# Performance work log

Measured on AMD Instinct MI355X. Metric: run time of the kernel, lower is better.

Reference implementation:

```python
import jax, jax.numpy as jnp
import numpy as np

N_ENT = 50000
N_EDGE = 500000
H_DIM = 128
N_REL_TAB = 475  # 2*n_rel + 1


def setup_inputs() -> dict:
    key = jax.random.key(0)
    ks = jax.random.split(key, 8)
    scale = 1.0 / np.sqrt(H_DIM)
    return {
        "ent_emb": jax.random.normal(ks[0], (N_ENT, H_DIM), jnp.float32) * scale,
        "rel_emb": jax.random.normal(ks[1], (N_REL_TAB, H_DIM), jnp.float32) * scale,
        "w_edge": jax.random.normal(ks[2], (H_DIM, H_DIM), jnp.float32) * scale,
        "w_node": jax.random.normal(ks[3], (H_DIM, H_DIM), jnp.float32) * scale,
        "w_comp": jax.random.normal(ks[4], (H_DIM, H_DIM), jnp.float32) * scale,
        "src": jax.random.randint(ks[5], (N_EDGE,), 0, N_ENT, jnp.int32),
        "dst": jax.random.randint(ks[6], (N_EDGE,), 0, N_ENT, jnp.int32),
        "rel_id": jax.random.randint(ks[7], (N_EDGE,), 0, N_REL_TAB - 1, jnp.int32),
    }


def _edge_softmax(logits, dst, n_nodes):
    # dgl.ops.edge_softmax: softmax over incoming edges of each destination node
    m = jax.ops.segment_max(logits, dst, num_segments=n_nodes)  # (N,)
    ex = jnp.exp(logits - m[dst])                               # (E,)
    s = jax.ops.segment_sum(ex, dst, num_segments=n_nodes)     # (N,)
    return ex / s[dst]


def _attn_aggregate(msg, key_emb_dst, dst, n_nodes, w):
    # norm = e_dot_v, edge_softmax, weighted scatter-sum, GEMM, Tanh
    logits = jnp.sum(msg * key_emb_dst, axis=-1)                # (E,)
    a = _edge_softmax(logits, dst, n_nodes)                     # (E,)
    neigh = jax.ops.segment_sum(msg * a[:, None], dst, num_segments=n_nodes)  # (N,H)
    return jnp.tanh(neigh @ w)


def reference(ent_emb, rel_emb, w_edge, w_node, w_comp, src, dst, rel_id):
    n = ent_emb.shape[0]
    v = ent_emb[dst]            # (E,H) destination node emb (shared key for all layers)
    u = ent_emb[src]            # (E,H)
    r = rel_emb[rel_id]         # (E,H)

    # EdgeLayer: message = rel emb
    edge_out = _attn_aggregate(r, v, dst, n, w_edge)
    # NodeLayer: message = src node emb (u_dot_v logits, u_mul_e aggregation)
    node_out = _attn_aggregate(u, v, dst, n, w_node)
    # CompLayer (comp_op='add'): message = u + rel emb
    comp_out = _attn_aggregate(u + r, v, dst, n, w_comp)

    return ent_emb + edge_out + node_out + comp_out
```

## Files before the change

kernel.cpp:

```cpp
#include <hip/hip_runtime.h>
#include <math.h>

#define N_ENT   50000
#define N_REL   475
#define N_EDGE  500000
#define HD      128

typedef unsigned int u32;
typedef __attribute__((ext_vector_type(8))) short short8;
typedef __attribute__((ext_vector_type(4))) float f32x4;
typedef __attribute__((ext_vector_type(4))) u32 u32x4;

__device__ __forceinline__ u32 bf16_1(float f) {
  u32 u = __float_as_uint(f);
  return (u + 0x7fffu + ((u >> 16) & 1u)) >> 16;
}
__device__ __forceinline__ u32 bf16_pack(float lo, float hi) {
  return bf16_1(lo) | (bf16_1(hi) << 16);
}
__device__ __forceinline__ float bf_lo(u32 w) { return __uint_as_float(w << 16); }
__device__ __forceinline__ float bf_hi(u32 w) { return __uint_as_float(w & 0xffff0000u); }
__device__ __forceinline__ float fast_tanh(float x) {
  float e = __expf(2.f * x);
  return 1.f - 2.f * __builtin_amdgcn_rcpf(e + 1.f);
}

__global__ void k_degree(const int* __restrict__ dst, int* __restrict__ counts) {
  int e = blockIdx.x * 256 + threadIdx.x;
  if (e < N_EDGE) atomicAdd(&counts[dst[e]], 1);
}

__global__ void k_blocksum(const int* __restrict__ counts, int* __restrict__ bsum) {
  __shared__ int sh[256];
  int i = blockIdx.x * 256 + threadIdx.x;
  sh[threadIdx.x] = (i < N_ENT) ? counts[i] : 0;
  __syncthreads();
  for (int off = 128; off > 0; off >>= 1) {
    if (threadIdx.x < off) sh[threadIdx.x] += sh[threadIdx.x + off];
    __syncthreads();
  }
  if (threadIdx.x == 0) bsum[blockIdx.x] = sh[0];
}

__global__ void k_scan_top(int* __restrict__ bsum, int nb) {
  __shared__ int sh[256];
  int t = threadIdx.x;
  int v = (t < nb) ? bsum[t] : 0;
  sh[t] = v;
  __syncthreads();
  for (int off = 1; off < 256; off <<= 1) {
    int x = (t >= off) ? sh[t - off] : 0;
    __syncthreads();
    sh[t] += x;
    __syncthreads();
  }
  if (t < nb) bsum[t] = sh[t] - v;
}

__global__ void k_scan_final(const int* __restrict__ counts, const int* __restrict__ bsum,
                             int* __restrict__ row_ptr) {
  __shared__ int sh[256];
  int t = threadIdx.x;
  int i = blockIdx.x * 256 + t;
  int v = (i < N_ENT) ? counts[i] : 0;
  sh[t] = v;
  __syncthreads();
  for (int off = 1; off < 256; off <<= 1) {
    int x = (t >= off) ? sh[t - off] : 0;
    __syncthreads();
    sh[t] += x;
    __syncthreads();
  }
  if (i < N_ENT) row_ptr[i] = sh[t] - v + bsum[blockIdx.x];
  if (i == N_ENT - 1) row_ptr[N_ENT] = N_EDGE;
}

__global__ void k_scatter(const int* __restrict__ src, const int* __restrict__ dst,
                          const int* __restrict__ rel, const int* __restrict__ row_ptr,
                          int* __restrict__ cursor, u32* __restrict__ psru) {
  int e = blockIdx.x * 256 + threadIdx.x;
  if (e >= N_EDGE) return;
  int d = dst[e];
  int pos = row_ptr[d] + atomicAdd(&cursor[d], 1);
  psru[pos] = (u32)src[e] | ((u32)rel[e] << 16);
}

__global__ void k_cvt_pack(const float* __restrict__ ent, const float* __restrict__ rel,
                           const float* __restrict__ we, const float* __restrict__ wn,
                           const float* __restrict__ wc, u32* __restrict__ ent16,
                           u32* __restrict__ rel16, u32* __restrict__ wpack) {
  const int CVT = (N_ENT + N_REL) * 16;
  int t = blockIdx.x * 256 + threadIdx.x;
  if (t < CVT) {
    int row = t >> 4, seg = t & 15;
    const float* s;
    u32* d;
    if (row < N_ENT) {
      s = ent + (size_t)row * HD + seg * 8;
      d = ent16 + (size_t)row * 64 + seg * 4;
    } else {
      int rr = row - N_ENT;
      s = rel + (size_t)rr * HD + seg * 8;
      d = rel16 + (size_t)rr * 64 + seg * 4;
    }
    float4 A = *(const float4*)s, B = *(const float4*)(s + 4);
    u32x4 o = {bf16_pack(A.x, A.y), bf16_pack(A.z, A.w),
               bf16_pack(B.x, B.y), bf16_pack(B.z, B.w)};
    *(u32x4*)d = o;
  } else if (t < CVT + 3 * 8 * 4 * 64) {
    int idx = t - CVT;
    int lane = idx & 63, ks = (idx >> 6) & 3, ct = (idx >> 8) & 7, l = idx >> 11;
    const float* W = (l == 0) ? we : (l == 1) ? wn : wc;
    int c = ct * 16 + (lane & 15);
    int kb = ks * 32 + (lane >> 4) * 8;
    u32x4 o;
#pragma unroll
    for (int jp = 0; jp < 4; ++jp) {
      int k0 = kb + 2 * jp;
      o[jp] = bf16_pack(W[k0 * HD + c], W[(k0 + 1) * HD + c]);
    }
    *(u32x4*)(wpack + idx * 4) = o;
  }
}

__global__ __launch_bounds__(256) void k_aggregate(
    const float* __restrict__ ent, const u32* __restrict__ ent16,
    const u32* __restrict__ rel16, const int* __restrict__ row_ptr,
    const u32* __restrict__ psru, u32* __restrict__ neighb) {
  int lane = threadIdx.x & 63;
  int node = blockIdx.x * 4 + (threadIdx.x >> 6);
  int grp = lane >> 4, gl = lane & 15;

  const float* vp = ent + (size_t)node * HD + gl * 8;
  float4 va = *(const float4*)vp, vb = *(const float4*)(vp + 4);
  float vv[8] = {va.x, va.y, va.z, va.w, vb.x, vb.y, vb.z, vb.w};

  float S0 = 0.f, S1 = 0.f, S2 = 0.f;
  float a0[8], a1[8], a2[8];
#pragma unroll
  for (int j = 0; j < 8; ++j) a0[j] = a1[j] = a2[j] = 0.f;

  int e0 = row_ptr[node], e1 = row_ptr[node + 1];
  if (e0 < e1) {
    int elast = e1 - 1;
    auto fetch = [&](int eb, u32x4& U, u32x4& R) {
      int e = eb + grp;
      u32 p = psru[(e < e1) ? e : elast];
      U = *(const u32x4*)(ent16 + (size_t)(p & 0xFFFFu) * 64 + gl * 4);
      R = *(const u32x4*)(rel16 + (size_t)(p >> 16) * 64 + gl * 4);
    };
    auto process = [&](u32x4& U, u32x4& R, int eb) {
      float cu[8], cr[8];
#pragma unroll
      for (int k = 0; k < 4; ++k) {
        cu[2 * k] = bf_lo(U[k]); cu[2 * k + 1] = bf_hi(U[k]);
        cr[2 * k] = bf_lo(R[k]); cr[2 * k + 1] = bf_hi(R[k]);
      }
      if (eb + 8 < e1) fetch(eb + 8, U, R);
      bool valid = (eb + grp < e1);
      float pu = 0.f, pq = 0.f;
#pragma unroll
      for (int j = 0; j < 8; ++j) {
        pu = fmaf(cu[j], vv[j], pu);
        pq = fmaf(cr[j], vv[j], pq);
      }
#pragma unroll
      for (int off = 1; off < 16; off <<= 1) {
        pu += __shfl_xor(pu, off, 64);
        pq += __shfl_xor(pq, off, 64);
      }
      float e_u = valid ? __expf(pu) : 0.f;
      float e_r = valid ? __expf(pq) : 0.f;
      float e_c = e_u * e_r;
      S0 += e_r; S1 += e_u; S2 += e_c;
#pragma unroll
      for (int j = 0; j < 8; ++j) {
        a0[j] = fmaf(e_r, cr[j], a0[j]);
        a1[j] = fmaf(e_u, cu[j], a1[j]);
        a2[j] = fmaf(e_c, cu[j] + cr[j], a2[j]);
      }
    };
    u32x4 uA, rA, uB, rB;
    fetch(e0, uA, rA);
    if (e0 + 4 < e1) fetch(e0 + 4, uB, rB);
    for (int eb = e0; eb < e1; eb += 8) {
      process(uA, rA, eb);
      if (eb + 4 < e1) process(uB, rB, eb + 4);
    }
  }

  S0 += __shfl_xor(S0, 16, 64); S0 += __shfl_xor(S0, 32, 64);
  S1 += __shfl_xor(S1, 16, 64); S1 += __shfl_xor(S1, 32, 64);
  S2 += __shfl_xor(S2, 16, 64); S2 += __shfl_xor(S2, 32, 64);
  float w0 = (S0 > 0.f) ? __builtin_amdgcn_rcpf(S0) : 0.f;
  float w1 = (S1 > 0.f) ? __builtin_amdgcn_rcpf(S1) : 0.f;
  float w2 = (S2 > 0.f) ? __builtin_amdgcn_rcpf(S2) : 0.f;
#pragma unroll
  for (int j = 0; j < 8; ++j) {
    a0[j] += __shfl_xor(a0[j], 16, 64); a0[j] += __shfl_xor(a0[j], 32, 64);
    a1[j] += __shfl_xor(a1[j], 16, 64); a1[j] += __shfl_xor(a1[j], 32, 64);
    a2[j] += __shfl_xor(a2[j], 16, 64); a2[j] += __shfl_xor(a2[j], 32, 64);
  }

  int base = node * 64 + gl * 4;
  if (grp == 0) {
    u32x4 o = {bf16_pack(a0[0] * w0, a0[1] * w0), bf16_pack(a0[2] * w0, a0[3] * w0),
               bf16_pack(a0[4] * w0, a0[5] * w0), bf16_pack(a0[6] * w0, a0[7] * w0)};
    *(u32x4*)(neighb + base) = o;
  } else if (grp == 1) {
    u32x4 o = {bf16_pack(a1[0] * w1, a1[1] * w1), bf16_pack(a1[2] * w1, a1[3] * w1),
               bf16_pack(a1[4] * w1, a1[5] * w1), bf16_pack(a1[6] * w1, a1[7] * w1)};
    *(u32x4*)(neighb + N_ENT * 64 + base) = o;
  } else if (grp == 2) {
    u32x4 o = {bf16_pack(a2[0] * w2, a2[1] * w2), bf16_pack(a2[2] * w2, a2[3] * w2),
               bf16_pack(a2[4] * w2, a2[5] * w2), bf16_pack(a2[6] * w2, a2[7] * w2)};
    *(u32x4*)(neighb + 2 * N_ENT * 64 + base) = o;
  }
}

__global__ __launch_bounds__(256) void k_out(
    const float* __restrict__ ent, const u32* __restrict__ neighb,
    const u32* __restrict__ wpack, float* __restrict__ out) {
  int lane = threadIdx.x & 63, wv = threadIdx.x >> 6;
  int n0 = blockIdx.x * 64 + wv * 16;

  int arow = n0 + (lane & 15);
  int arow_c = (arow < N_ENT) ? arow : 0;
  int ko2 = (lane >> 4) * 4;

  f32x4 res[8];
#pragma unroll
  for (int t = 0; t < 8; ++t) res[t] = (f32x4){0.f, 0.f, 0.f, 0.f};

#pragma unroll
  for (int l = 0; l < 3; ++l) {
    const u32* nb = neighb + (size_t)l * N_ENT * 64;
    short8 a[4];
#pragma unroll
    for (int ks = 0; ks < 4; ++ks)
      a[ks] = *(const short8*)(nb + (size_t)arow_c * 64 + ks * 16 + ko2);
    const u32* wp = wpack + l * 8192;
#pragma unroll
    for (int ct = 0; ct < 8; ++ct) {
      f32x4 acc = (f32x4){0.f, 0.f, 0.f, 0.f};
#pragma unroll
      for (int ks = 0; ks < 4; ++ks) {
        short8 b = *(const short8*)(wp + ((ct * 4 + ks) * 64 + lane) * 4);
        acc = __builtin_amdgcn_mfma_f32_16x16x32_bf16(a[ks], b, acc, 0, 0, 0);
      }
#pragma unroll
      for (int r = 0; r < 4; ++r) res[ct][r] += fast_tanh(acc[r]);
    }
  }
  int rbase = n0 + (lane >> 4) * 4;
  int cbase = lane & 15;
#pragma unroll
  for (int ct = 0; ct < 8; ++ct) {
    int col = ct * 16 + cbase;
#pragma unroll
    for (int r = 0; r < 4; ++r) {
      int row = rbase + r;
      if (row < N_ENT)
        out[(size_t)row * HD + col] = ent[(size_t)row * HD + col] + res[ct][r];
    }
  }
}

extern "C" void kernel_launch(void* const* d_in, const int* in_sizes, int n_in,
                              void* d_out, int out_size, void* d_ws, size_t ws_size,
                              hipStream_t stream) {
  const float* ent = (const float*)d_in[0];
  const float* rel = (const float*)d_in[1];
  const float* w_e = (const float*)d_in[2];
  const float* w_n = (const float*)d_in[3];
  const float* w_c = (const float*)d_in[4];
  const int* src = (const int*)d_in[5];
  const int* dst = (const int*)d_in[6];
  const int* relid = (const int*)d_in[7];
  float* out = (float*)d_out;

  char* ws = (char*)d_ws;
  size_t off = 0;
  auto alloc = [&](size_t bytes) {
    void* p = ws + off;
    off = (off + bytes + 255) & ~(size_t)255;
    return p;
  };
  int* counts = (int*)alloc((size_t)N_ENT * 4);
  int* cursor = (int*)alloc((size_t)N_ENT * 4);
  int* row_ptr = (int*)alloc((size_t)(N_ENT + 1) * 4);
  int* bsum = (int*)alloc(256 * 4);
  u32* psru = (u32*)alloc((size_t)N_EDGE * 4);
  u32* ent16 = (u32*)alloc((size_t)N_ENT * 64 * 4);
  u32* rel16 = (u32*)alloc((size_t)N_REL * 64 * 4);
  u32* neighb = (u32*)alloc(3ull * N_ENT * 64 * 4);
  u32* wpack = (u32*)alloc((size_t)3 * 8 * 4 * 64 * 4 * 4);
  (void)ws_size; (void)in_sizes; (void)n_in; (void)out_size;

  hipMemsetAsync(counts, 0, (size_t)((char*)row_ptr - (char*)counts), stream);

  int nb = (N_ENT + 255) / 256;
  k_degree<<<(N_EDGE + 255) / 256, 256, 0, stream>>>(dst, counts);
  k_blocksum<<<nb, 256, 0, stream>>>(counts, bsum);
  k_scan_top<<<1, 256, 0, stream>>>(bsum, nb);
  k_scan_final<<<nb, 256, 0, stream>>>(counts, bsum, row_ptr);
  k_scatter<<<(N_EDGE + 255) / 256, 256, 0, stream>>>(src, dst, relid, row_ptr, cursor,
                                                      psru);
  const int CVTN = (N_ENT + N_REL) * 16 + 3 * 8 * 4 * 64;
  k_cvt_pack<<<(CVTN + 255) / 256, 256, 0, stream>>>(ent, rel, w_e, w_n, w_c, ent16,
                                                     rel16, wpack);
  k_aggregate<<<N_ENT / 4, 256, 0, stream>>>(ent, ent16, rel16, row_ptr, psru, neighb);
  k_out<<<(N_ENT + 63) / 64, 256, 0, stream>>>(ent, neighb, wpack, out);
}
```

Before: 245.2 us.

## Fuse degree count with bf16 conversion and deepen aggregate prefetch with packed math

The degree-count and bf16 conversion/weight-pack kernels are merged into one launch, which saves a launch and lets the two independent jobs overlap. The aggregate kernel now reads the destination key from the bf16 table instead of fp32 and uses three prefetch buffers instead of two. Its arithmetic is rewritten with float2 vectors so the compiler can emit packed FMA. The fetch for eb+12 has no guard, but it clamps to the last edge, and the key now carries bf16 rounding, which slightly changes precision.

```diff
diff --git a/kernel.cpp b/kernel.cpp
--- a/kernel.cpp
+++ b/kernel.cpp
@@ -9,6 +9,7 @@
 typedef unsigned int u32;
 typedef __attribute__((ext_vector_type(8))) short short8;
 typedef __attribute__((ext_vector_type(4))) float f32x4;
+typedef __attribute__((ext_vector_type(2))) float f32x2;
 typedef __attribute__((ext_vector_type(4))) u32 u32x4;
 
 __device__ __forceinline__ u32 bf16_1(float f) {
@@ -20,77 +21,29 @@
 }
 __device__ __forceinline__ float bf_lo(u32 w) { return __uint_as_float(w << 16); }
 __device__ __forceinline__ float bf_hi(u32 w) { return __uint_as_float(w & 0xffff0000u); }
+__device__ __forceinline__ f32x2 bf2(u32 w) { return (f32x2){bf_lo(w), bf_hi(w)}; }
 __device__ __forceinline__ float fast_tanh(float x) {
   float e = __expf(2.f * x);
   return 1.f - 2.f * __builtin_amdgcn_rcpf(e + 1.f);
 }
 
-__global__ void k_degree(const int* __restrict__ dst, int* __restrict__ counts) {
-  int e = blockIdx.x * 256 + threadIdx.x;
-  if (e < N_EDGE) atomicAdd(&counts[dst[e]], 1);
-}
-
-__global__ void k_blocksum(const int* __restrict__ counts, int* __restrict__ bsum) {
-  __shared__ int sh[256];
-  int i = blockIdx.x * 256 + threadIdx.x;
-  sh[threadIdx.x] = (i < N_ENT) ? counts[i] : 0;
-  __syncthreads();
-  for (int off = 128; off > 0; off >>= 1) {
-    if (threadIdx.x < off) sh[threadIdx.x] += sh[threadIdx.x + off];
-    __syncthreads();
-  }
-  if (threadIdx.x == 0) bsum[blockIdx.x] = sh[0];
-}
-
-__global__ void k_scan_top(int* __restrict__ bsum, int nb) {
-  __shared__ int sh[256];
-  int t = threadIdx.x;
-  int v = (t < nb) ? bsum[t] : 0;
-  sh[t] = v;
-  __syncthreads();
-  for (int off = 1; off < 256; off <<= 1) {
-    int x = (t >= off) ? sh[t - off] : 0;
-    __syncthreads();
-    sh[t] += x;
-    __syncthreads();
-  }
-  if (t < nb) bsum[t] = sh[t] - v;
-}
-
-__global__ void k_scan_final(const int* __restrict__ counts, const int* __restrict__ bsum,
-                             int* __restrict__ row_ptr) {
-  __shared__ int sh[256];
-  int t = threadIdx.x;
-  int i = blockIdx.x * 256 + t;
-  int v = (i < N_ENT) ? counts[i] : 0;
-  sh[t] = v;
-  __syncthreads();
-  for (int off = 1; off < 256; off <<= 1) {
-    int x = (t >= off) ? sh[t - off] : 0;
-    __syncthreads();
-    sh[t] += x;
-    __syncthreads();
-  }
-  if (i < N_ENT) row_ptr[i] = sh[t] - v + bsum[blockIdx.x];
-  if (i == N_ENT - 1) row_ptr[N_ENT] = N_EDGE;
-}
-
-__global__ void k_scatter(const int* __restrict__ src, const int* __restrict__ dst,
-                          const int* __restrict__ rel, const int* __restrict__ row_ptr,
-                          int* __restrict__ cursor, u32* __restrict__ psru) {
-  int e = blockIdx.x * 256 + threadIdx.x;
-  if (e >= N_EDGE) return;
-  int d = dst[e];
-  int pos = row_ptr[d] + atomicAdd(&cursor[d], 1);
-  psru[pos] = (u32)src[e] | ((u32)rel[e] << 16);
-}
-
-__global__ void k_cvt_pack(const float* __restrict__ ent, const float* __restrict__ rel,
-                           const float* __restrict__ we, const float* __restrict__ wn,
-                           const float* __restrict__ wc, u32* __restrict__ ent16,
-                           u32* __restrict__ rel16, u32* __restrict__ wpack) {
+#define DEG_BLKS ((N_EDGE + 255) / 256)
+#define CVT_ITEMS ((N_ENT + N_REL) * 16 + 3 * 8 * 4 * 64)
+#define CVT_BLKS ((CVT_ITEMS + 255) / 256)
+
+__global__ void k_degree_cvt(const int* __restrict__ dst, int* __restrict__ counts,
+                             const float* __restrict__ ent, const float* __restrict__ rel,
+                             const float* __restrict__ we, const float* __restrict__ wn,
+                             const float* __restrict__ wc, u32* __restrict__ ent16,
+                             u32* __restrict__ rel16, u32* __restrict__ wpack) {
+  int b = blockIdx.x;
+  if (b < DEG_BLKS) {
+    int e = b * 256 + threadIdx.x;
+    if (e < N_EDGE) atomicAdd(&counts[dst[e]], 1);
+    return;
+  }
+  int t = (b - DEG_BLKS) * 256 + threadIdx.x;
   const int CVT = (N_ENT + N_REL) * 16;
-  int t = blockIdx.x * 256 + threadIdx.x;
   if (t < CVT) {
     int row = t >> 4, seg = t & 15;
     const float* s;
@@ -107,7 +60,7 @@
     u32x4 o = {bf16_pack(A.x, A.y), bf16_pack(A.z, A.w),
                bf16_pack(B.x, B.y), bf16_pack(B.z, B.w)};
     *(u32x4*)d = o;
-  } else if (t < CVT + 3 * 8 * 4 * 64) {
+  } else if (t < CVT_ITEMS) {
     int idx = t - CVT;
     int lane = idx & 63, ks = (idx >> 6) & 3, ct = (idx >> 8) & 7, l = idx >> 11;
     const float* W = (l == 0) ? we : (l == 1) ? wn : wc;
@@ -123,22 +76,79 @@
   }
 }
 
+__global__ void k_blocksum(const int* __restrict__ counts, int* __restrict__ bsum) {
+  __shared__ int sh[256];
+  int i = blockIdx.x * 256 + threadIdx.x;
+  sh[threadIdx.x] = (i < N_ENT) ? counts[i] : 0;
+  __syncthreads();
+  for (int off = 128; off > 0; off >>= 1) {
+    if (threadIdx.x < off) sh[threadIdx.x] += sh[threadIdx.x + off];
+    __syncthreads();
+  }
+  if (threadIdx.x == 0) bsum[blockIdx.x] = sh[0];
+}
+
+__global__ void k_scan_top(int* __restrict__ bsum, int nb) {
+  __shared__ int sh[256];
+  int t = threadIdx.x;
+  int v = (t < nb) ? bsum[t] : 0;
+  sh[t] = v;
+  __syncthreads();
+  for (int off = 1; off < 256; off <<= 1) {
+    int x = (t >= off) ? sh[t - off] : 0;
+    __syncthreads();
+    sh[t] += x;
+    __syncthreads();
+  }
+  if (t < nb) bsum[t] = sh[t] - v;
+}
+
+__global__ void k_scan_final(const int* __restrict__ counts, const int* __restrict__ bsum,
+                             int* __restrict__ row_ptr) {
+  __shared__ int sh[256];
+  int t = threadIdx.x;
+  int i = blockIdx.x * 256 + t;
+  int v = (i < N_ENT) ? counts[i] : 0;
+  sh[t] = v;
+  __syncthreads();
+  for (int off = 1; off < 256; off <<= 1) {
+    int x = (t >= off) ? sh[t - off] : 0;
+    __syncthreads();
+    sh[t] += x;
+    __syncthreads();
+  }
+  if (i < N_ENT) row_ptr[i] = sh[t] - v + bsum[blockIdx.x];
+  if (i == N_ENT - 1) row_ptr[N_ENT] = N_EDGE;
+}
+
+__global__ void k_scatter(const int* __restrict__ src, const int* __restrict__ dst,
+                          const int* __restrict__ rel, const int* __restrict__ row_ptr,
+                          int* __restrict__ cursor, u32* __restrict__ psru) {
+  int e = blockIdx.x * 256 + threadIdx.x;
+  if (e >= N_EDGE) return;
+  int d = dst[e];
+  int pos = row_ptr[d] + atomicAdd(&cursor[d], 1);
+  psru[pos] = (u32)src[e] | ((u32)rel[e] << 16);
+}
+
 __global__ __launch_bounds__(256) void k_aggregate(
-    const float* __restrict__ ent, const u32* __restrict__ ent16,
-    const u32* __restrict__ rel16, const int* __restrict__ row_ptr,
-    const u32* __restrict__ psru, u32* __restrict__ neighb) {
+    const u32* __restrict__ ent16, const u32* __restrict__ rel16,
+    const int* __restrict__ row_ptr, const u32* __restrict__ psru,
+    u32* __restrict__ neighb) {
   int lane = threadIdx.x & 63;
   int node = blockIdx.x * 4 + (threadIdx.x >> 6);
   int grp = lane >> 4, gl = lane & 15;
 
-  const float* vp = ent + (size_t)node * HD + gl * 8;
-  float4 va = *(const float4*)vp, vb = *(const float4*)(vp + 4);
-  float vv[8] = {va.x, va.y, va.z, va.w, vb.x, vb.y, vb.z, vb.w};
-
-  float S0 = 0.f, S1 = 0.f, S2 = 0.f;
-  float a0[8], a1[8], a2[8];
-#pragma unroll
-  for (int j = 0; j < 8; ++j) a0[j] = a1[j] = a2[j] = 0.f;
+  u32x4 V = *(const u32x4*)(ent16 + (size_t)node * 64 + gl * 4);
+  f32x2 vv2[4];
+#pragma unroll
+  for (int k = 0; k < 4; ++k) vv2[k] = bf2(V[k]);
+
+  f32x2 Su = {0.f, 0.f};
+  float S2 = 0.f;
+  f32x2 a0[4], a1[4], a2[4];
+#pragma unroll
+  for (int k = 0; k < 4; ++k) a0[k] = a1[k] = a2[k] = (f32x2){0.f, 0.f};
 
   int e0 = row_ptr[node], e1 = row_ptr[node + 1];
   if (e0 < e1) {
@@ -150,70 +160,84 @@
       R = *(const u32x4*)(rel16 + (size_t)(p >> 16) * 64 + gl * 4);
     };
     auto process = [&](u32x4& U, u32x4& R, int eb) {
-      float cu[8], cr[8];
+      f32x2 cu2[4], cr2[4];
+#pragma unroll
+      for (int k = 0; k < 4; ++k) { cu2[k] = bf2(U[k]); cr2[k] = bf2(R[k]); }
+      fetch(eb + 12, U, R);
+      bool valid = (eb + grp < e1);
+      f32x2 du2 = {0.f, 0.f}, dq2 = {0.f, 0.f};
 #pragma unroll
       for (int k = 0; k < 4; ++k) {
-        cu[2 * k] = bf_lo(U[k]); cu[2 * k + 1] = bf_hi(U[k]);
-        cr[2 * k] = bf_lo(R[k]); cr[2 * k + 1] = bf_hi(R[k]);
+        du2 += cu2[k] * vv2[k];
+        dq2 += cr2[k] * vv2[k];
       }
-      if (eb + 8 < e1) fetch(eb + 8, U, R);
-      bool valid = (eb + grp < e1);
-      float pu = 0.f, pq = 0.f;
-#pragma unroll
-      for (int j = 0; j < 8; ++j) {
-        pu = fmaf(cu[j], vv[j], pu);
-        pq = fmaf(cr[j], vv[j], pq);
+      f32x2 p = {du2.x + du2.y, dq2.x + dq2.y};
+#pragma unroll
+      for (int off = 1; off < 16; off <<= 1) {
+        f32x2 t;
+        t.x = __shfl_xor(p.x, off, 64);
+        t.y = __shfl_xor(p.y, off, 64);
+        p += t;
       }
-#pragma unroll
-      for (int off = 1; off < 16; off <<= 1) {
-        pu += __shfl_xor(pu, off, 64);
-        pq += __shfl_xor(pq, off, 64);
-      }
-      float e_u = valid ? __expf(pu) : 0.f;
-      float e_r = valid ? __expf(pq) : 0.f;
+      float e_u = valid ? __expf(p.x) : 0.f;
+      float e_r = valid ? __expf(p.y) : 0.f;
       float e_c = e_u * e_r;
-      S0 += e_r; S1 += e_u; S2 += e_c;
-#pragma unroll
-      for (int j = 0; j < 8; ++j) {
-        a0[j] = fmaf(e_r, cr[j], a0[j]);
-        a1[j] = fmaf(e_u, cu[j], a1[j]);
-        a2[j] = fmaf(e_c, cu[j] + cr[j], a2[j]);
+      Su += (f32x2){e_r, e_u};
+      S2 += e_c;
+      f32x2 er2 = {e_r, e_r}, eu2 = {e_u, e_u}, ec2 = {e_c, e_c};
+#pragma unroll
+      for (int k = 0; k < 4; ++k) {
+        a0[k] += er2 * cr2[k];
+        a1[k] += eu2 * cu2[k];
+        a2[k] += ec2 * (cu2[k] + cr2[k]);
       }
     };
-    u32x4 uA, rA, uB, rB;
+    u32x4 uA, rA, uB, rB, uC, rC;
     fetch(e0, uA, rA);
-    if (e0 + 4 < e1) fetch(e0 + 4, uB, rB);
-    for (int eb = e0; eb < e1; eb += 8) {
+    fetch(e0 + 4, uB, rB);
+    fetch(e0 + 8, uC, rC);
+    int eb = e0;
+    for (; eb + 8 < e1; eb += 12) {
       process(uA, rA, eb);
-      if (eb + 4 < e1) process(uB, rB, eb + 4);
-    }
-  }
-
-  S0 += __shfl_xor(S0, 16, 64); S0 += __shfl_xor(S0, 32, 64);
-  S1 += __shfl_xor(S1, 16, 64); S1 += __shfl_xor(S1, 32, 64);
-  S2 += __shfl_xor(S2, 16, 64); S2 += __shfl_xor(S2, 32, 64);
-  float w0 = (S0 > 0.f) ? __builtin_amdgcn_rcpf(S0) : 0.f;
-  float w1 = (S1 > 0.f) ? __builtin_amdgcn_rcpf(S1) : 0.f;
+      process(uB, rB, eb + 4);
+      process(uC, rC, eb + 8);
+    }
+    if (eb < e1) process(uA, rA, eb);
+    if (eb + 4 < e1) process(uB, rB, eb + 4);
+  }
+
+  {
+    f32x2 t;
+    t.x = __shfl_xor(Su.x, 16, 64); t.y = __shfl_xor(Su.y, 16, 64); Su += t;
+    t.x = __shfl_xor(Su.x, 32, 64); t.y = __shfl_xor(Su.y, 32, 64); Su += t;
+    S2 += __shfl_xor(S2, 16, 64); S2 += __shfl_xor(S2, 32, 64);
+  }
+  float w0 = (Su.x > 0.f) ? __builtin_amdgcn_rcpf(Su.x) : 0.f;
+  float w1 = (Su.y > 0.f) ? __builtin_amdgcn_rcpf(Su.y) : 0.f;
   float w2 = (S2 > 0.f) ? __builtin_amdgcn_rcpf(S2) : 0.f;
 #pragma unroll
-  for (int j = 0; j < 8; ++j) {
-    a0[j] += __shfl_xor(a0[j], 16, 64); a0[j] += __shfl_xor(a0[j], 32, 64);
-    a1[j] += __shfl_xor(a1[j], 16, 64); a1[j] += __shfl_xor(a1[j], 32, 64);
-    a2[j] += __shfl_xor(a2[j], 16, 64); a2[j] += __shfl_xor(a2[j], 32, 64);
+  for (int k = 0; k < 4; ++k) {
+    f32x2 t;
+    t.x = __shfl_xor(a0[k].x, 16, 64); t.y = __shfl_xor(a0[k].y, 16, 64); a0[k] += t;
+    t.x = __shfl_xor(a0[k].x, 32, 64); t.y = __shfl_xor(a0[k].y, 32, 64); a0[k] += t;
+    t.x = __shfl_xor(a1[k].x, 16, 64); t.y = __shfl_xor(a1[k].y, 16, 64); a1[k] += t;
+    t.x = __shfl_xor(a1[k].x, 32, 64); t.y = __shfl_xor(a1[k].y, 32, 64); a1[k] += t;
+    t.x = __shfl_xor(a2[k].x, 16, 64); t.y = __shfl_xor(a2[k].y, 16, 64); a2[k] += t;
+    t.x = __shfl_xor(a2[k].x, 32, 64); t.y = __shfl_xor(a2[k].y, 32, 64); a2[k] += t;
   }
 
   int base = node * 64 + gl * 4;
   if (grp == 0) {
-    u32x4 o = {bf16_pack(a0[0] * w0, a0[1] * w0), bf16_pack(a0[2] * w0, a0[3] * w0),
-               bf16_pack(a0[4] * w0, a0[5] * w0), bf16_pack(a0[6] * w0, a0[7] * w0)};
+    u32x4 o = {bf16_pack(a0[0].x * w0, a0[0].y * w0), bf16_pack(a0[1].x * w0, a0[1].y * w0),
+               bf16_pack(a0[2].x * w0, a0[2].y * w0), bf16_pack(a0[3].x * w0, a0[3].y * w0)};
     *(u32x4*)(neighb + base) = o;
   } else if (grp == 1) {
-    u32x4 o = {bf16_pack(a1[0] * w1, a1[1] * w1), bf16_pack(a1[2] * w1, a1[3] * w1),
-               bf16_pack(a1[4] * w1, a1[5] * w1), bf16_pack(a1[6] * w1, a1[7] * w1)};
+    u32x4 o = {bf16_pack(a1[0].x * w1, a1[0].y * w1), bf16_pack(a1[1].x * w1, a1[1].y * w1),
+               bf16_pack(a1[2].x * w1, a1[2].y * w1), bf16_pack(a1[3].x * w1, a1[3].y * w1)};
     *(u32x4*)(neighb + N_ENT * 64 + base) = o;
   } else if (grp == 2) {
-    u32x4 o = {bf16_pack(a2[0] * w2, a2[1] * w2), bf16_pack(a2[2] * w2, a2[3] * w2),
-               bf16_pack(a2[4] * w2, a2[5] * w2), bf16_pack(a2[6] * w2, a2[7] * w2)};
+    u32x4 o = {bf16_pack(a2[0].x * w2, a2[0].y * w2), bf16_pack(a2[1].x * w2, a2[1].y * w2),
+               bf16_pack(a2[2].x * w2, a2[2].y * w2), bf16_pack(a2[3].x * w2, a2[3].y * w2)};
     *(u32x4*)(neighb + 2 * N_ENT * 64 + base) = o;
   }
 }
@@ -300,15 +324,13 @@
   hipMemsetAsync(counts, 0, (size_t)((char*)row_ptr - (char*)counts), stream);
 
   int nb = (N_ENT + 255) / 256;
-  k_degree<<<(N_EDGE + 255) / 256, 256, 0, stream>>>(dst, counts);
+  k_degree_cvt<<<DEG_BLKS + CVT_BLKS, 256, 0, stream>>>(dst, counts, ent, rel, w_e, w_n,
+                                                        w_c, ent16, rel16, wpack);
   k_blocksum<<<nb, 256, 0, stream>>>(counts, bsum);
   k_scan_top<<<1, 256, 0, stream>>>(bsum, nb);
   k_scan_final<<<nb, 256, 0, stream>>>(counts, bsum, row_ptr);
   k_scatter<<<(N_EDGE + 255) / 256, 256, 0, stream>>>(src, dst, relid, row_ptr, cursor,
                                                       psru);
-  const int CVTN = (N_ENT + N_REL) * 16 + 3 * 8 * 4 * 64;
-  k_cvt_pack<<<(CVTN + 255) / 256, 256, 0, stream>>>(ent, rel, w_e, w_n, w_c, ent16,
-                                                     rel16, wpack);
-  k_aggregate<<<N_ENT / 4, 256, 0, stream>>>(ent, ent16, rel16, row_ptr, psru, neighb);
+  k_aggregate<<<N_ENT / 4, 256, 0, stream>>>(ent16, rel16, row_ptr, psru, neighb);
   k_out<<<(N_ENT + 63) / 64, 256, 0, stream>>>(ent, neighb, wpack, out);
 }
```

Result: no change. 241.4 us (-1.5%).
